# Optimization experiments

Hardware: AMD Instinct MI355X
Metric: run time of the kernel (lower is better)

Reference implementation:

```python
import jax, jax.numpy as jnp
import numpy as np

# max_valences dict {0:4,1:3,2:2,3:6,4:1,5:1,6:1,7:1,8:4,9:4,10:4}, default 4
MAX_VALENCES = jnp.array([4, 3, 2, 6, 1, 1, 1, 1, 4, 4, 4], dtype=jnp.float32)
DEFAULT_VALENCE = 4.0


def setup_inputs() -> dict:
    N, E, D = 500000, 16000000, 128
    key = jax.random.key(0)
    k1, k2, k3, k4 = jax.random.split(key, 4)
    h = jax.random.normal(k1, (N, D), dtype=jnp.float32)
    edge_index = jax.random.randint(k2, (2, E), 0, N, dtype=jnp.int64)
    predicted_valences = jax.random.uniform(k3, (N,), dtype=jnp.float32) * 4.0
    atom_types = jax.random.randint(k4, (N,), 0, 11, dtype=jnp.int64)
    return {"h": h, "edge_index": edge_index,
            "predicted_valences": predicted_valences, "atom_types": atom_types}


def reference(h, edge_index, predicted_valences, atom_types):
    N = h.shape[0]
    row = edge_index[0]
    # bond_counts.index_add_(0, row, ones)  ->  scatter-add of ones over source nodes
    bond_counts = jnp.zeros((N,), dtype=h.dtype).at[row].add(jnp.ones_like(row, dtype=h.dtype))
    # vectorized dict lookup: max_valences.get(atom_type, 4)
    in_table = (atom_types >= 0) & (atom_types < MAX_VALENCES.shape[0])
    idx = jnp.clip(atom_types, 0, MAX_VALENCES.shape[0] - 1)
    max_allowed = jnp.where(in_table, MAX_VALENCES[idx], DEFAULT_VALENCE)
    # violation only where bond_count > max_allowed
    violation = jnp.maximum(bond_counts - max_allowed, 0.0)
    violations = jnp.sum(violation * violation) / N
    h_out = h * (1.0 - 0.1 * violation)[:, None]
    return h_out, violations
```

## Files before the change

### kernel.cpp

```cpp
#include <hip/hip_runtime.h>
#include <math.h>

__constant__ float c_maxv[11] = {4.f, 3.f, 2.f, 6.f, 1.f, 1.f, 1.f, 1.f, 4.f, 4.f, 4.f};

#define NREP 8
#define RSHIFT 11
#define RANGE 2048
#define EPB 8192
#define BPAD 256


__global__ __launch_bounds__(256)
void scatter_kernel(const int* __restrict__ row, unsigned short* __restrict__ seg,
                    unsigned int* __restrict__ gcursor, int E, int CAP) {
    __shared__ unsigned int hist[BPAD];
    __shared__ unsigned int scn[BPAD];
    __shared__ unsigned int place[BPAD];
    __shared__ unsigned int gbase[BPAD];
    __shared__ int sbuf[EPB];

    const int tid = threadIdx.x;
    const int base = blockIdx.x * EPB;
    const int nvalid = min(EPB, E - base);
    const bool full = (nvalid == EPB);

    hist[tid] = 0;
    __syncthreads();

    int vals[32];
    if (full) {
        #pragma unroll
        for (int k = 0; k < 8; ++k) {
            int4 r = reinterpret_cast<const int4*>(row + base)[k * 256 + tid];
            vals[4*k+0] = r.x; vals[4*k+1] = r.y; vals[4*k+2] = r.z; vals[4*k+3] = r.w;
        }
        #pragma unroll
        for (int k = 0; k < 32; ++k)
            atomicAdd(&hist[((unsigned)vals[k]) >> RSHIFT], 1u);
    } else {
        for (int i = tid; i < nvalid; i += 256)
            atomicAdd(&hist[((unsigned)row[base + i]) >> RSHIFT], 1u);
    }
    __syncthreads();

    const unsigned int mycnt = hist[tid];
    gbase[tid] = atomicAdd(&gcursor[tid], mycnt);
    scn[tid] = mycnt;
    __syncthreads();
    #pragma unroll
    for (int off = 1; off < BPAD; off <<= 1) {
        unsigned int v = (tid >= off) ? scn[tid - off] : 0u;
        __syncthreads();
        scn[tid] += v;
        __syncthreads();
    }
    place[tid] = scn[tid] - mycnt;
    __syncthreads();

    if (full) {
        #pragma unroll
        for (int k = 0; k < 32; ++k) {
            int v = vals[k];
            unsigned int p = atomicAdd(&place[((unsigned)v) >> RSHIFT], 1u);
            sbuf[p] = v;
        }
    } else {
        for (int i = tid; i < nvalid; i += 256) {
            int v = row[base + i];
            unsigned int p = atomicAdd(&place[((unsigned)v) >> RSHIFT], 1u);
            sbuf[p] = v;
        }
    }
    __syncthreads();

    for (int i = tid; i < nvalid; i += 256) {
        int v = sbuf[i];
        int b = ((unsigned)v) >> RSHIFT;
        unsigned int ofs = scn[b] - hist[b];
        unsigned int pos = gbase[b] + ((unsigned)i - ofs);
        if (pos < (unsigned)CAP)
            seg[(size_t)b * (size_t)CAP + pos] = (unsigned short)(v & (RANGE - 1));
    }
}

__global__ __launch_bounds__(256)
void bucket_kernel(const unsigned short* __restrict__ seg,
                   const unsigned int* __restrict__ gcursor,
                   const int* __restrict__ atom_types,
                   float* __restrict__ sarr, float* __restrict__ viol,
                   int N, int CAP, float inv_n) {
    __shared__ unsigned int h2[RANGE];
    const int tid = threadIdx.x;
    const int b = blockIdx.x;

    #pragma unroll
    for (int j = 0; j < RANGE / 256; ++j) h2[tid + j * 256] = 0;
    __syncthreads();

    unsigned int cnt = gcursor[b];
    if (cnt > (unsigned)CAP) cnt = (unsigned)CAP;
    const unsigned short* s = seg + (size_t)b * (size_t)CAP;

    const uint2* s4 = (const uint2*)s;
    unsigned int n4 = cnt >> 2;
    for (unsigned int i = tid; i < n4; i += 256) {
        uint2 w = s4[i];
        atomicAdd(&h2[w.x & 0xffffu], 1u);
        atomicAdd(&h2[w.x >> 16], 1u);
        atomicAdd(&h2[w.y & 0xffffu], 1u);
        atomicAdd(&h2[w.y >> 16], 1u);
    }
    for (unsigned int i = (n4 << 2) + tid; i < cnt; i += 256)
        atomicAdd(&h2[s[i]], 1u);
    __syncthreads();

    float local = 0.0f;
    const int rbase = b << RSHIFT;
    #pragma unroll
    for (int j = 0; j < RANGE / 256; ++j) {
        int idx = tid + j * 256;
        int r = rbase + idx;
        if (r < N) {
            float c = (float)h2[idx];
            int t = atom_types[r];
            float maxv = ((unsigned)t < 11u) ? c_maxv[t] : 4.0f;
            float v = fmaxf(c - maxv, 0.0f);
            sarr[r] = 1.0f - 0.1f * v;
            local += v * v;
        }
    }
    for (int off = 32; off > 0; off >>= 1)
        local += __shfl_down(local, off, 64);
    __shared__ float sred[4];
    if ((tid & 63) == 0) sred[tid >> 6] = local;
    __syncthreads();
    if (tid == 0)
        atomicAdd(viol, (sred[0] + sred[1] + sred[2] + sred[3]) * inv_n);
}


__global__ __launch_bounds__(256) void count_kernel(const int* __restrict__ row,
                                                    unsigned int* __restrict__ counts,
                                                    int nvec, int E, int N) {
    unsigned int* my = counts + (size_t)(blockIdx.x & (NREP - 1)) * (size_t)N;
    int i = blockIdx.x * 256 + threadIdx.x;
    if (i < nvec) {
        int4 r = reinterpret_cast<const int4*>(row)[i];
        atomicAdd(&my[r.x], 1u);
        atomicAdd(&my[r.y], 1u);
        atomicAdd(&my[r.z], 1u);
        atomicAdd(&my[r.w], 1u);
    }
    int e = nvec * 4 + i;
    if (e < E) atomicAdd(&my[row[e]], 1u);
}

__global__ __launch_bounds__(256) void node_kernel(const unsigned int* __restrict__ counts,
                                                   const int* __restrict__ atom_types,
                                                   float* __restrict__ sarr,
                                                   float* __restrict__ viol,
                                                   int N, float inv_n) {
    int stride = gridDim.x * 256;
    float local = 0.0f;
    for (int r = blockIdx.x * 256 + threadIdx.x; r < N; r += stride) {
        unsigned int c = 0;
        #pragma unroll
        for (int k = 0; k < NREP; ++k) c += counts[(size_t)k * (size_t)N + r];
        int t = atom_types[r];
        float maxv = (t >= 0 && t < 11) ? c_maxv[t] : 4.0f;
        float v = fmaxf((float)c - maxv, 0.0f);
        sarr[r] = 1.0f - 0.1f * v;
        local += v * v;
    }
    for (int off = 32; off > 0; off >>= 1)
        local += __shfl_down(local, off, 64);
    __shared__ float sdata[4];
    if ((threadIdx.x & 63) == 0) sdata[threadIdx.x >> 6] = local;
    __syncthreads();
    if (threadIdx.x == 0)
        atomicAdd(viol, (sdata[0] + sdata[1] + sdata[2] + sdata[3]) * inv_n);
}


__global__ __launch_bounds__(256) void scale_kernel(const float4* __restrict__ h,
                                                    const float* __restrict__ sarr,
                                                    float4* __restrict__ out,
                                                    int total, int cpr_shift) {
    int stride = gridDim.x * 256;
    for (int idx = blockIdx.x * 256 + threadIdx.x; idx < total; idx += stride) {
        float s = sarr[idx >> cpr_shift];
        float4 hv = h[idx];
        hv.x *= s; hv.y *= s; hv.z *= s; hv.w *= s;
        out[idx] = hv;
    }
}

extern "C" void kernel_launch(void* const* d_in, const int* in_sizes, int n_in,
                              void* d_out, int out_size, void* d_ws, size_t ws_size,
                              hipStream_t stream) {
    const float* h          = (const float*)d_in[0];
    const int*   edge       = (const int*)d_in[1];
    const int*   atom_types = (const int*)d_in[3];

    int N = in_sizes[3];
    int D = in_sizes[0] / N;
    int E = in_sizes[1] / 2;

    float* out  = (float*)d_out;
    float* viol = out + (size_t)N * (size_t)D;
    hipMemsetAsync(viol, 0, sizeof(float), stream);

    int B = (N + RANGE - 1) >> RSHIFT;

    double mean = (double)E * (double)RANGE / (double)N;
    int CAP = (int)(mean + 16.0 * sqrt(mean > 1.0 ? mean : 1.0) + 1024.0);
    CAP = (CAP + 63) & ~63;

    size_t seg_bytes = ((size_t)B * (size_t)CAP * 2 + 255) & ~(size_t)255;
    size_t need_new  = seg_bytes + 1024 + (size_t)N * 4;

    float* sarr;
    if (B <= BPAD && ws_size >= need_new) {
        unsigned short* seg     = (unsigned short*)d_ws;
        unsigned int*   gcursor = (unsigned int*)((char*)d_ws + seg_bytes);
        sarr = (float*)((char*)d_ws + seg_bytes + 1024);

        hipMemsetAsync(gcursor, 0, BPAD * sizeof(unsigned int), stream);

        int sblocks = (E + EPB - 1) / EPB;
        scatter_kernel<<<sblocks, 256, 0, stream>>>(edge, seg, gcursor, E, CAP);
        bucket_kernel<<<B, 256, 0, stream>>>(seg, gcursor, atom_types, sarr, viol,
                                             N, CAP, 1.0f / (float)N);
    } else {
        unsigned int* counts = (unsigned int*)d_ws;
        sarr = (float*)((char*)d_ws + (size_t)NREP * N * 4);
        hipMemsetAsync(counts, 0, (size_t)NREP * N * sizeof(unsigned int), stream);
        int nvec = E / 4;
        int cblocks = (nvec + 255) / 256;
        count_kernel<<<cblocks, 256, 0, stream>>>(edge, counts, nvec, E, N);
        node_kernel<<<512, 256, 0, stream>>>(counts, atom_types, sarr, viol, N,
                                             1.0f / (float)N);
    }

    int cpr = D / 4;
    int cpr_shift = 0; while ((1 << cpr_shift) < cpr) ++cpr_shift;
    int total = N * cpr;
    scale_kernel<<<8192, 256, 0, stream>>>((const float4*)h, sarr,
                                           (float4*)out, total, cpr_shift);
}
```

Baseline: 547.1 us.

## Fuse bucket histogram with row scaling and use wave-shuffle scan in scatter

Merges the per-bucket histogram/violation kernel with the h-scaling pass, so each 1024-thread block scales its own 2048 rows from shared memory. This removes the separate scale kernel launch and the sarr global round-trip. The violation total is accumulated in workspace and written by the last block via a done counter, which replaces a memset. The scatter kernel's block scan now uses wave shuffles instead of a barrier-heavy shared-memory scan, and the big streams use nontemporal loads and stores. A risk is that only 245 blocks now carry the whole 256 MB scaling pass, which may underuse the GPU's bandwidth.

```diff
diff --git a/kernel.cpp b/kernel.cpp
--- a/kernel.cpp
+++ b/kernel.cpp
@@ -8,6 +8,9 @@
 #define RANGE 2048
 #define EPB 8192
 #define BPAD 256
+
+typedef float f4 __attribute__((ext_vector_type(4)));
+typedef int   i4 __attribute__((ext_vector_type(4)));
 
 
 __global__ __launch_bounds__(256)
@@ -17,6 +20,7 @@
     __shared__ unsigned int scn[BPAD];
     __shared__ unsigned int place[BPAD];
     __shared__ unsigned int gbase[BPAD];
+    __shared__ unsigned int wtot[4];
     __shared__ int sbuf[EPB];
 
     const int tid = threadIdx.x;
@@ -31,7 +35,8 @@
     if (full) {
         #pragma unroll
         for (int k = 0; k < 8; ++k) {
-            int4 r = reinterpret_cast<const int4*>(row + base)[k * 256 + tid];
+            i4 r = __builtin_nontemporal_load(
+                reinterpret_cast<const i4*>(row + base) + k * 256 + tid);
             vals[4*k+0] = r.x; vals[4*k+1] = r.y; vals[4*k+2] = r.z; vals[4*k+3] = r.w;
         }
         #pragma unroll
@@ -45,56 +50,66 @@
 
     const unsigned int mycnt = hist[tid];
     gbase[tid] = atomicAdd(&gcursor[tid], mycnt);
-    scn[tid] = mycnt;
-    __syncthreads();
+
+    unsigned int v = mycnt;
     #pragma unroll
-    for (int off = 1; off < BPAD; off <<= 1) {
-        unsigned int v = (tid >= off) ? scn[tid - off] : 0u;
-        __syncthreads();
-        scn[tid] += v;
-        __syncthreads();
-    }
-    place[tid] = scn[tid] - mycnt;
+    for (int off = 1; off < 64; off <<= 1) {
+        unsigned int n = __shfl_up(v, off, 64);
+        if ((tid & 63) >= off) v += n;
+    }
+    if ((tid & 63) == 63) wtot[tid >> 6] = v;
+    __syncthreads();
+    unsigned int wofs = 0;
+    #pragma unroll
+    for (int w = 0; w < 4; ++w) wofs += (w < (tid >> 6)) ? wtot[w] : 0u;
+    unsigned int inc = v + wofs;
+    scn[tid] = inc;
+    place[tid] = inc - mycnt;
     __syncthreads();
 
     if (full) {
         #pragma unroll
         for (int k = 0; k < 32; ++k) {
-            int v = vals[k];
-            unsigned int p = atomicAdd(&place[((unsigned)v) >> RSHIFT], 1u);
-            sbuf[p] = v;
+            int x = vals[k];
+            unsigned int p = atomicAdd(&place[((unsigned)x) >> RSHIFT], 1u);
+            sbuf[p] = x;
         }
     } else {
         for (int i = tid; i < nvalid; i += 256) {
-            int v = row[base + i];
-            unsigned int p = atomicAdd(&place[((unsigned)v) >> RSHIFT], 1u);
-            sbuf[p] = v;
-        }
-    }
+            int x = row[base + i];
+            unsigned int p = atomicAdd(&place[((unsigned)x) >> RSHIFT], 1u);
+            sbuf[p] = x;
+        }
+    }
+    __syncthreads();
+    hist[tid] = scn[tid] - hist[tid];
     __syncthreads();
 
     for (int i = tid; i < nvalid; i += 256) {
-        int v = sbuf[i];
-        int b = ((unsigned)v) >> RSHIFT;
-        unsigned int ofs = scn[b] - hist[b];
-        unsigned int pos = gbase[b] + ((unsigned)i - ofs);
+        int x = sbuf[i];
+        int b = ((unsigned)x) >> RSHIFT;
+        unsigned int pos = gbase[b] + ((unsigned)i - hist[b]);
         if (pos < (unsigned)CAP)
-            seg[(size_t)b * (size_t)CAP + pos] = (unsigned short)(v & (RANGE - 1));
-    }
-}
-
-__global__ __launch_bounds__(256)
-void bucket_kernel(const unsigned short* __restrict__ seg,
-                   const unsigned int* __restrict__ gcursor,
-                   const int* __restrict__ atom_types,
-                   float* __restrict__ sarr, float* __restrict__ viol,
-                   int N, int CAP, float inv_n) {
+            seg[(size_t)b * (size_t)CAP + pos] = (unsigned short)(x & (RANGE - 1));
+    }
+}
+
+__global__ __launch_bounds__(1024)
+void fused_kernel(const unsigned short* __restrict__ seg,
+                  const unsigned int* __restrict__ gcursor,
+                  const int* __restrict__ atom_types,
+                  const float* __restrict__ h, float* __restrict__ out,
+                  float* __restrict__ viol_out, float* __restrict__ vz,
+                  unsigned int* __restrict__ done,
+                  int N, int CAP, float inv_n, int nblocks) {
     __shared__ unsigned int h2[RANGE];
+    __shared__ float svals[RANGE];
+    __shared__ float sred[16];
+
     const int tid = threadIdx.x;
     const int b = blockIdx.x;
 
-    #pragma unroll
-    for (int j = 0; j < RANGE / 256; ++j) h2[tid + j * 256] = 0;
+    h2[tid] = 0; h2[tid + 1024] = 0;
     __syncthreads();
 
     unsigned int cnt = gcursor[b];
@@ -103,39 +118,71 @@
 
     const uint2* s4 = (const uint2*)s;
     unsigned int n4 = cnt >> 2;
-    for (unsigned int i = tid; i < n4; i += 256) {
+    for (unsigned int i = tid; i < n4; i += 1024) {
         uint2 w = s4[i];
         atomicAdd(&h2[w.x & 0xffffu], 1u);
         atomicAdd(&h2[w.x >> 16], 1u);
         atomicAdd(&h2[w.y & 0xffffu], 1u);
         atomicAdd(&h2[w.y >> 16], 1u);
     }
-    for (unsigned int i = (n4 << 2) + tid; i < cnt; i += 256)
+    for (unsigned int i = (n4 << 2) + tid; i < cnt; i += 1024)
         atomicAdd(&h2[s[i]], 1u);
     __syncthreads();
 
+    const int rbase = b << RSHIFT;
+    const int nr = min(RANGE, N - rbase);
     float local = 0.0f;
-    const int rbase = b << RSHIFT;
     #pragma unroll
-    for (int j = 0; j < RANGE / 256; ++j) {
-        int idx = tid + j * 256;
+    for (int j = 0; j < 2; ++j) {
+        int idx = tid + j * 1024;
         int r = rbase + idx;
         if (r < N) {
             float c = (float)h2[idx];
             int t = atom_types[r];
             float maxv = ((unsigned)t < 11u) ? c_maxv[t] : 4.0f;
-            float v = fmaxf(c - maxv, 0.0f);
-            sarr[r] = 1.0f - 0.1f * v;
-            local += v * v;
-        }
-    }
+            float vv = fmaxf(c - maxv, 0.0f);
+            svals[idx] = 1.0f - 0.1f * vv;
+            local += vv * vv;
+        }
+    }
+    __syncthreads();
+
+    const f4* h4 = reinterpret_cast<const f4*>(h);
+    f4* o4 = reinterpret_cast<f4*>(out);
+    const size_t g4 = (size_t)rbase * 32;
+    const int t4 = nr * 32;
+    int i = tid;
+    for (; i + 1024 < t4; i += 2048) {
+        f4 a = __builtin_nontemporal_load(h4 + g4 + i);
+        f4 c = __builtin_nontemporal_load(h4 + g4 + i + 1024);
+        float sa = svals[i >> 5];
+        float sc = svals[(i + 1024) >> 5];
+        a *= sa;
+        c *= sc;
+        __builtin_nontemporal_store(a, o4 + g4 + i);
+        __builtin_nontemporal_store(c, o4 + g4 + i + 1024);
+    }
+    for (; i < t4; i += 1024) {
+        f4 a = __builtin_nontemporal_load(h4 + g4 + i);
+        float sa = svals[i >> 5];
+        a *= sa;
+        __builtin_nontemporal_store(a, o4 + g4 + i);
+    }
+
     for (int off = 32; off > 0; off >>= 1)
         local += __shfl_down(local, off, 64);
-    __shared__ float sred[4];
     if ((tid & 63) == 0) sred[tid >> 6] = local;
     __syncthreads();
-    if (tid == 0)
-        atomicAdd(viol, (sred[0] + sred[1] + sred[2] + sred[3]) * inv_n);
+    if (tid == 0) {
+        float ssum = 0.0f;
+        #pragma unroll
+        for (int k = 0; k < 16; ++k) ssum += sred[k];
+        atomicAdd(vz, ssum * inv_n);
+        __threadfence();
+        unsigned int t = atomicAdd(done, 1u);
+        if (t == (unsigned)(nblocks - 1))
+            *viol_out = atomicAdd(vz, 0.0f);
+    }
 }
 
 
@@ -181,7 +228,6 @@
         atomicAdd(viol, (sdata[0] + sdata[1] + sdata[2] + sdata[3]) * inv_n);
 }
 
-
 __global__ __launch_bounds__(256) void scale_kernel(const float4* __restrict__ h,
                                                     const float* __restrict__ sarr,
                                                     float4* __restrict__ out,
@@ -208,7 +254,6 @@
 
     float* out  = (float*)d_out;
     float* viol = out + (size_t)N * (size_t)D;
-    hipMemsetAsync(viol, 0, sizeof(float), stream);
 
     int B = (N + RANGE - 1) >> RSHIFT;
 
@@ -217,34 +262,36 @@
     CAP = (CAP + 63) & ~63;
 
     size_t seg_bytes = ((size_t)B * (size_t)CAP * 2 + 255) & ~(size_t)255;
-    size_t need_new  = seg_bytes + 1024 + (size_t)N * 4;
-
-    float* sarr;
-    if (B <= BPAD && ws_size >= need_new) {
+    size_t ctl_bytes = (size_t)BPAD * 4 + 64;
+    size_t need_new  = seg_bytes + ctl_bytes;
+
+    if (B <= BPAD && D == 128 && ws_size >= need_new) {
         unsigned short* seg     = (unsigned short*)d_ws;
         unsigned int*   gcursor = (unsigned int*)((char*)d_ws + seg_bytes);
-        sarr = (float*)((char*)d_ws + seg_bytes + 1024);
-
-        hipMemsetAsync(gcursor, 0, BPAD * sizeof(unsigned int), stream);
+        float*          vz      = (float*)((char*)d_ws + seg_bytes + (size_t)BPAD * 4);
+        unsigned int*   done    = (unsigned int*)(vz + 1);
+
+        (void)hipMemsetAsync(gcursor, 0, ctl_bytes, stream);
 
         int sblocks = (E + EPB - 1) / EPB;
         scatter_kernel<<<sblocks, 256, 0, stream>>>(edge, seg, gcursor, E, CAP);
-        bucket_kernel<<<B, 256, 0, stream>>>(seg, gcursor, atom_types, sarr, viol,
-                                             N, CAP, 1.0f / (float)N);
+        fused_kernel<<<B, 1024, 0, stream>>>(seg, gcursor, atom_types,
+                                             h, out, viol, vz, done, N, CAP,
+                                             1.0f / (float)N, B);
     } else {
         unsigned int* counts = (unsigned int*)d_ws;
-        sarr = (float*)((char*)d_ws + (size_t)NREP * N * 4);
-        hipMemsetAsync(counts, 0, (size_t)NREP * N * sizeof(unsigned int), stream);
+        float* sarr = (float*)((char*)d_ws + (size_t)NREP * N * 4);
+        (void)hipMemsetAsync(counts, 0, (size_t)NREP * N * sizeof(unsigned int), stream);
+        (void)hipMemsetAsync(viol, 0, sizeof(float), stream);
         int nvec = E / 4;
         int cblocks = (nvec + 255) / 256;
         count_kernel<<<cblocks, 256, 0, stream>>>(edge, counts, nvec, E, N);
         node_kernel<<<512, 256, 0, stream>>>(counts, atom_types, sarr, viol, N,
                                              1.0f / (float)N);
-    }
-
-    int cpr = D / 4;
-    int cpr_shift = 0; while ((1 << cpr_shift) < cpr) ++cpr_shift;
-    int total = N * cpr;
-    scale_kernel<<<8192, 256, 0, stream>>>((const float4*)h, sarr,
-                                           (float4*)out, total, cpr_shift);
-}
+        int cpr = D / 4;
+        int cpr_shift = 0; while ((1 << cpr_shift) < cpr) ++cpr_shift;
+        int total = N * cpr;
+        scale_kernel<<<8192, 256, 0, stream>>>((const float4*)h, sarr,
+                                               (float4*)out, total, cpr_shift);
+    }
+}
```

Measured after the change: 535.6 us. 1.02x faster.
